# Optimization experiments

Measured on AMD Instinct MI355X. Metric: run time of the kernel, lower is better.

The kernel has to match this reference:

```python
import jax, jax.numpy as jnp
import numpy as np


def _chain_edges(n):
    # bidirectional chain edges + self loops (PyG GATConv add_self_loops=True default)
    src = np.concatenate([np.arange(n - 1), np.arange(1, n), np.arange(n)])
    dst = np.concatenate([np.arange(1, n), np.arange(n - 1), np.arange(n)])
    return jnp.asarray(src), jnp.asarray(dst)


def _gat(x, W, a_src, a_dst, bias, src, dst, n, heads, ch, concat):
    # x: [B, n, Fin]; PyG GATConv v1 math (lin has no bias, bias added post-agg)
    B = x.shape[0]
    xh = (x @ W).reshape(B, n, heads, ch)  # [B,n,h,c]
    es = jnp.einsum('bnhc,hc->bnh', xh, a_src)
    ed = jnp.einsum('bnhc,hc->bnh', xh, a_dst)
    e = jax.nn.leaky_relu(es[:, src] + ed[:, dst], 0.2)  # [B,E,h]
    e = jnp.moveaxis(e, 1, 0)                            # [E,B,h]
    m = jax.ops.segment_max(e, dst, num_segments=n)      # scatter-softmax over incoming edges
    w = jnp.exp(e - m[dst])
    denom = jax.ops.segment_sum(w, dst, num_segments=n)
    alpha = w / denom[dst]                               # [E,B,h]
    msgs = alpha[..., None] * jnp.moveaxis(xh[:, src], 1, 0)  # [E,B,h,c]
    out = jnp.moveaxis(jax.ops.segment_sum(msgs, dst, num_segments=n), 0, 1)  # [B,n,h,c]
    out = out.reshape(B, n, heads * ch) if concat else out.mean(axis=2)
    return out + bias


def _mlp(x, w1, b1, w2, b2, w3, b3):
    h = jax.nn.leaky_relu(x @ w1 + b1, 0.01)
    h = jax.nn.leaky_relu(h @ w2 + b2, 0.01)
    return h @ w3 + b3


def setup_inputs() -> dict:
    key = jax.random.key(0)
    ks = jax.random.split(key, 21)
    B, n, d_state, hid, da = 2048, 50, 64, 128, 4
    r = lambda k, shp, s: (jax.random.normal(k, shp, dtype=jnp.float32) * s)
    return {
        'state': r(ks[0], (B, n, d_state), 1.0),
        'W1': r(ks[1], (d_state, 2 * hid), 0.1), 'att_src1': r(ks[2], (2, hid), 0.1),
        'att_dst1': r(ks[3], (2, hid), 0.1), 'b1': r(ks[4], (2 * hid,), 0.02),
        'W2': r(ks[5], (2 * hid, hid), 0.1), 'att_src2': r(ks[6], (1, hid), 0.1),
        'att_dst2': r(ks[7], (1, hid), 0.1), 'b2': r(ks[8], (hid,), 0.02),
        'aw1': r(ks[9], (hid, 128), 0.1), 'ab1': r(ks[10], (128,), 0.02),
        'aw2': r(ks[11], (128, 128), 0.1), 'ab2': r(ks[12], (128,), 0.02),
        'aw3': r(ks[13], (128, da), 0.1), 'ab3': r(ks[14], (da,), 0.02),
        'vw1': r(ks[15], (hid, 128), 0.1), 'vb1': r(ks[16], (128,), 0.02),
        'vw2': r(ks[17], (128, 128), 0.1), 'vb2': r(ks[18], (128,), 0.02),
        'vw3': r(ks[19], (128, 1), 0.1), 'vb3': r(ks[20], (1,), 0.02),
    }


def reference(state, W1, att_src1, att_dst1, b1, W2, att_src2, att_dst2, b2,
              aw1, ab1, aw2, ab2, aw3, ab3, vw1, vb1, vw2, vb2, vw3, vb3):
    B, n, _ = state.shape
    src, dst = _chain_edges(n)
    x = jax.nn.gelu(_gat(state, W1, att_src1, att_dst1, b1, src, dst, n, 2, 128, True), approximate=False)
    x = jax.nn.gelu(_gat(x, W2, att_src2, att_dst2, b2, src, dst, n, 1, 128, False), approximate=False)
    graph_emb = x.mean(axis=1)                      # global_mean_pool over chain nodes
    value = _mlp(graph_emb, vw1, vb1, vw2, vb2, vw3, vb3)   # [B,1]
    mean = _mlp(x, aw1, ab1, aw2, ab2, aw3, ab3).reshape(B, -1)  # [B, n*d_action]
    return mean, value
```

## Files before the change

kernel.cpp:

```cpp
#include <hip/hip_runtime.h>

#define DI __device__ __forceinline__

typedef unsigned int uint32;
typedef unsigned short u16;
typedef __attribute__((ext_vector_type(8))) short s8v;
typedef __attribute__((ext_vector_type(4))) float f4v;

DI float lrelu(float x, float s){ return x > 0.f ? x : s*x; }
DI u16 f2bu(float f){ uint32 u = __float_as_uint(f); return (u16)((u + 0x7FFFu + ((u>>16)&1u)) >> 16); }
DI float fastrcp(float x){ float r; asm("v_rcp_f32 %0, %1" : "=v"(r) : "v"(x)); return r; }

DI float gelu_f(float x){
  const float z = fabsf(x) * 0.70710678118654752f;
  const float t = fastrcp(1.f + 0.3275911f*z);
  float p = 1.061405429f;
  p = p*t - 1.453152027f;
  p = p*t + 1.421413741f;
  p = p*t - 0.284496736f;
  p = p*t + 0.254829592f;
  p = p*t;
  const float e = __expf(-z*z);
  float er = 1.f - p*e;
  er = copysignf(er, x);
  return 0.5f*x*(1.f + er);
}

DI f4v mfma16(s8v a, s8v b, f4v c){
  return __builtin_amdgcn_mfma_f32_16x16x32_bf16(a, b, c, 0, 0, 0);
}

constexpr int NNODE = 50;
constexpr int NT = 512;
constexpr int SCS = 134;

constexpr int WS1  = 0;
constexpr int WS2  = 18432;
constexpr int WSA1 = 55296;
constexpr int WSA2 = 71680;
constexpr int WSTOT= 88064;

__global__ __launch_bounds__(256)
void ac_prep(const float* __restrict__ w1, const float* __restrict__ as1, const float* __restrict__ ad1,
             const float* __restrict__ w2, const float* __restrict__ as2, const float* __restrict__ ad2,
             const float* __restrict__ aw1, const float* __restrict__ aw2, u16* __restrict__ ws)
{
  const int T1 = 2*144*64, T2 = 144*256, T3 = 128*128;
  for (int t = blockIdx.x*blockDim.x + threadIdx.x; t < WSTOT; t += gridDim.x*blockDim.x){
    float v; int o;
    if (t < T1){
      int h = t / 9216, r = t - h*9216, n = r>>6, k = r&63;
      if (n < 128) v = w1[k*256 + h*128 + n];
      else if (n < 130){
        const float* av = ((n==129) ? ad1 : as1) + h*128;
        const float* wr = w1 + k*256 + h*128;
        float s = 0.f;
        for (int c=0;c<128;++c) s += wr[c]*av[c];
        v = s;
      } else v = 0.f;
      o = WS1 + h*9216 + n*64 + k;
    } else if (t < T1+T2){
      int j = t - T1, n = j>>8, k = j&255;
      if (n < 128) v = w2[k*128 + n];
      else if (n < 130){
        const float* av = (n==129) ? ad2 : as2;
        const float* wr = w2 + k*128;
        float s = 0.f;
        for (int c=0;c<128;++c) s += wr[c]*av[c];
        v = s;
      } else v = 0.f;
      o = WS2 + n*256 + k;
    } else if (t < T1+T2+T3){
      int j = t - T1 - T2, n = j>>7, k = j&127;
      v = aw1[k*128 + n];
      o = WSA1 + n*128 + k;
    } else {
      int j = t - T1 - T2 - T3, n = j>>7, k = j&127;
      v = aw2[k*128 + n];
      o = WSA2 + n*128 + k;
    }
    ws[o] = f2bu(v);
  }
}


__global__ __launch_bounds__(NT, 4)
void ac_main(const float* __restrict__ state,
             const float* __restrict__ b1, const float* __restrict__ b2,
             const float* __restrict__ ab1, const float* __restrict__ ab2,
             const float* __restrict__ aw3, const float* __restrict__ ab3,
             const float* __restrict__ vw1, const float* __restrict__ vb1,
             const float* __restrict__ vw2, const float* __restrict__ vb2,
             const float* __restrict__ vw3, const float* __restrict__ vb3,
             const u16* __restrict__ ws,
             float* __restrict__ out_mean, float* __restrict__ out_val)
{
  __shared__ __align__(16) float sm[18816];
  float* sc   = sm;
  u16*   pAb  = (u16*)(sm + 8576);
  u16*   pAb2 = pAb + 8192;
  u16*   pAs  = (u16*)(sm + 16768);
  float* geb4 = sm + 16768;
  float* geb  = sm + 17280;
  float* vh1  = sm + 17408;

  const int tid = threadIdx.x, b = blockIdx.x;
  const int wid = tid>>6, l15 = tid&15, g = (tid>>4)&3;

  {
    const float4* xb4 = (const float4*)(state + (size_t)b * (NNODE*64));
    for (int t = tid; t < 800; t += NT){
      float4 v = xb4[t];
      int i = t>>4, k0 = (t&15)*4;
      ushort4 u;
      u.x = f2bu(v.x); u.y = f2bu(v.y); u.z = f2bu(v.z); u.w = f2bu(v.w);
      *(ushort4*)(pAs + i*64 + (k0 ^ ((i&7)<<3))) = u;
    }
    for (int t = tid; t < 224; t += NT){
      int i = 50 + (t>>4), k0 = (t&15)*4;
      *(ushort4*)(pAs + i*64 + (k0 ^ ((i&7)<<3))) = (ushort4){0,0,0,0};
    }
  }
  __syncthreads();

  {
    s8v aS[4][2];
    #pragma unroll
    for (int mt=0;mt<4;++mt)
      #pragma unroll
      for (int ks=0;ks<2;++ks){
        int row = mt*16 + l15, c = ks*32 + g*8;
        aS[mt][ks] = *(const s8v*)(pAs + row*64 + (c ^ ((row&7)<<3)));
      }

    for (int h=0; h<2; ++h){
      for (int nt = wid; nt < 9; nt += 8){
        f4v acc[4];
        #pragma unroll
        for (int mt=0;mt<4;++mt) acc[mt] = (f4v){0.f,0.f,0.f,0.f};
        #pragma unroll
        for (int ks=0;ks<2;++ks){
          s8v bf = *(const s8v*)(ws + WS1 + h*9216 + (nt*16 + l15)*64 + ks*32 + g*8);
          #pragma unroll
          for (int mt=0;mt<4;++mt) acc[mt] = mfma16(aS[mt][ks], bf, acc[mt]);
        }
        const int col = nt*16 + l15;
        if (col < 130){
          #pragma unroll
          for (int mt=0;mt<4;++mt){
            const int r0 = mt*16 + g*4;
            #pragma unroll
            for (int r=0;r<4;++r) sc[(r0+r)*SCS + col] = acc[mt][r];
          }
        }
      }
      __syncthreads();

      {
        const int base_j = h*128;
        #pragma unroll 4
        for (int t=0; t<13; ++t){
          const int c = tid + t*NT;
          if (c < 6400){
            const int i = c >> 7, j = c & 127;
            const float edi = sc[i*SCS + 129];
            const float cur = sc[i*SCS + j];
            const float pv  = (i > 0)        ? sc[(i-1)*SCS + j] : 0.f;
            const float nx  = (i < NNODE-1)  ? sc[(i+1)*SCS + j] : 0.f;
            const float esf = lrelu(sc[i*SCS + 128] + edi, 0.2f);
            float m = esf, el = 0.f, er = 0.f;
            if (i > 0)       { el = lrelu(sc[(i-1)*SCS + 128] + edi, 0.2f); m = fmaxf(m, el); }
            if (i < NNODE-1) { er = lrelu(sc[(i+1)*SCS + 128] + edi, 0.2f); m = fmaxf(m, er); }
            const float wS = __expf(esf - m);
            const float wL = (i > 0)       ? __expf(el - m) : 0.f;
            const float wR = (i < NNODE-1) ? __expf(er - m) : 0.f;
            const float agg = (wL*pv + wS*cur + wR*nx) * fastrcp(wL+wS+wR);
            const float v = gelu_f(agg + b1[base_j + j]);
            const int jj = base_j + j;
            pAb[i*256 + (jj ^ ((i&7)<<3))] = f2bu(v);
          }
        }
      }
      __syncthreads();
    }
  }

  for (int nt = wid; nt < 9; nt += 8){
    f4v acc[4];
    #pragma unroll
    for (int mt=0;mt<4;++mt) acc[mt] = (f4v){0.f,0.f,0.f,0.f};
    #pragma unroll
    for (int ks=0;ks<8;++ks){
      s8v bf = *(const s8v*)(ws + WS2 + (nt*16 + l15)*256 + ks*32 + g*8);
      #pragma unroll
      for (int mt=0;mt<4;++mt){
        const int row = mt*16 + l15, c = ks*32 + g*8;
        s8v a = *(const s8v*)(pAb + row*256 + (c ^ ((row&7)<<3)));
        acc[mt] = mfma16(a, bf, acc[mt]);
      }
    }
    const int col = nt*16 + l15;
    if (col < 130){
      #pragma unroll
      for (int mt=0;mt<4;++mt){
        const int r0 = mt*16 + g*4;
        #pragma unroll
        for (int r=0;r<4;++r) sc[(r0+r)*SCS + col] = acc[mt][r];
      }
    }
  }
  __syncthreads();

  {
    const int q = tid>>7, j = tid&127;
    const int i0 = q*13, i1 = (i0+13 < NNODE) ? i0+13 : NNODE;
    const float bj = b2[j];
    float ps = 0.f;
    #pragma unroll 4
    for (int i = i0; i < i1; ++i){
      const float edi = sc[i*SCS + 129];
      const float cur = sc[i*SCS + j];
      const float pv  = (i > 0)       ? sc[(i-1)*SCS + j] : 0.f;
      const float nx  = (i < NNODE-1) ? sc[(i+1)*SCS + j] : 0.f;
      const float esf = lrelu(sc[i*SCS + 128] + edi, 0.2f);
      float m = esf, el = 0.f, er = 0.f;
      if (i > 0)       { el = lrelu(sc[(i-1)*SCS + 128] + edi, 0.2f); m = fmaxf(m, el); }
      if (i < NNODE-1) { er = lrelu(sc[(i+1)*SCS + 128] + edi, 0.2f); m = fmaxf(m, er); }
      const float wS = __expf(esf - m);
      const float wL = (i > 0)       ? __expf(el - m) : 0.f;
      const float wR = (i < NNODE-1) ? __expf(er - m) : 0.f;
      const float agg = (wL*pv + wS*cur + wR*nx) * fastrcp(wL+wS+wR);
      const float v = gelu_f(agg + bj);
      pAb[i*128 + (j ^ ((i&7)<<3))] = f2bu(v);
      ps += v;
    }
    geb4[q*128 + j] = ps;
  }
  __syncthreads();

  {
    const int nt = wid;
    f4v acc[4];
    #pragma unroll
    for (int mt=0;mt<4;++mt) acc[mt] = (f4v){0.f,0.f,0.f,0.f};
    #pragma unroll
    for (int ks=0;ks<4;++ks){
      s8v bf = *(const s8v*)(ws + WSA1 + (nt*16 + l15)*128 + ks*32 + g*8);
      #pragma unroll
      for (int mt=0;mt<4;++mt){
        const int row = mt*16 + l15, c = ks*32 + g*8;
        s8v a = *(const s8v*)(pAb + row*128 + (c ^ ((row&7)<<3)));
        acc[mt] = mfma16(a, bf, acc[mt]);
      }
    }
    const int col = nt*16 + l15;
    const float bj = ab1[col];
    #pragma unroll
    for (int mt=0;mt<4;++mt){
      #pragma unroll
      for (int r=0;r<4;++r){
        const int row = mt*16 + g*4 + r;
        const float v = lrelu(acc[mt][r] + bj, 0.01f);
        pAb2[row*128 + (col ^ ((row&7)<<3))] = f2bu(v);
      }
    }
    if (tid < 128)
      geb[tid] = (geb4[tid] + geb4[128+tid] + geb4[256+tid] + geb4[384+tid]) * 0.02f;
  }
  __syncthreads();

  {
    const int nt = wid;
    f4v acc[4];
    #pragma unroll
    for (int mt=0;mt<4;++mt) acc[mt] = (f4v){0.f,0.f,0.f,0.f};
    #pragma unroll
    for (int ks=0;ks<4;++ks){
      s8v bf = *(const s8v*)(ws + WSA2 + (nt*16 + l15)*128 + ks*32 + g*8);
      #pragma unroll
      for (int mt=0;mt<4;++mt){
        const int row = mt*16 + l15, c = ks*32 + g*8;
        s8v a = *(const s8v*)(pAb2 + row*128 + (c ^ ((row&7)<<3)));
        acc[mt] = mfma16(a, bf, acc[mt]);
      }
    }
    const int col = nt*16 + l15;
    #pragma unroll
    for (int mt=0;mt<4;++mt){
      const int r0 = mt*16 + g*4;
      #pragma unroll
      for (int r=0;r<4;++r) sc[(r0+r)*SCS + col] = acc[mt][r];
    }
  }
  __syncthreads();

  if (tid < 200){
    const int i = tid>>2, m = tid&3;
    const float* scr = sc + i*SCS;
    float s0=0.f,s1=0.f,s2=0.f,s3=0.f;
    #pragma unroll 4
    for (int k=0;k<128;k+=4){
      s0 += lrelu(scr[k  ]+ab2[k  ],0.01f)*aw3[(k  )*4+m];
      s1 += lrelu(scr[k+1]+ab2[k+1],0.01f)*aw3[(k+1)*4+m];
      s2 += lrelu(scr[k+2]+ab2[k+2],0.01f)*aw3[(k+2)*4+m];
      s3 += lrelu(scr[k+3]+ab2[k+3],0.01f)*aw3[(k+3)*4+m];
    }
    out_mean[(size_t)b*200 + i*4 + m] = (s0+s1)+(s2+s3) + ab3[m];
  } else if (tid >= 256 && tid < 384){
    const int j = tid - 256;
    float a0=0.f, a1=0.f;
    #pragma unroll 4
    for (int k=0;k<128;k+=2){
      a0 += geb[k  ]*vw1[(k  )*128 + j];
      a1 += geb[k+1]*vw1[(k+1)*128 + j];
    }
    vh1[j] = lrelu(a0+a1 + vb1[j], 0.01f);
  }
  __syncthreads();

  if (tid < 64){
    const int j = tid;
    float a0=0.f, c0=0.f;
    #pragma unroll 4
    for (int k=0;k<128;++k){
      const float gk = vh1[k];
      a0 += gk*vw2[k*128 + j];
      c0 += gk*vw2[k*128 + j + 64];
    }
    const float va = lrelu(a0 + vb2[j],    0.01f);
    const float vb = lrelu(c0 + vb2[j+64], 0.01f);
    float p = va*vw3[j] + vb*vw3[j+64];
    #pragma unroll
    for (int off=32; off>0; off>>=1) p += __shfl_down(p, off);
    if (j == 0) out_val[b] = p + vb3[0];
  }
}

extern "C" void kernel_launch(void* const* d_in, const int* in_sizes, int n_in,
                              void* d_out, int out_size, void* d_ws, size_t ws_size,
                              hipStream_t stream)
{
  const float* state = (const float*)d_in[0];
  const float* w1    = (const float*)d_in[1];
  const float* as1   = (const float*)d_in[2];
  const float* ad1   = (const float*)d_in[3];
  const float* b1_   = (const float*)d_in[4];
  const float* w2    = (const float*)d_in[5];
  const float* as2   = (const float*)d_in[6];
  const float* ad2   = (const float*)d_in[7];
  const float* b2_   = (const float*)d_in[8];
  const float* aw1   = (const float*)d_in[9];
  const float* ab1   = (const float*)d_in[10];
  const float* aw2   = (const float*)d_in[11];
  const float* ab2   = (const float*)d_in[12];
  const float* aw3   = (const float*)d_in[13];
  const float* ab3   = (const float*)d_in[14];
  const float* vw1   = (const float*)d_in[15];
  const float* vb1   = (const float*)d_in[16];
  const float* vw2   = (const float*)d_in[17];
  const float* vb2   = (const float*)d_in[18];
  const float* vw3   = (const float*)d_in[19];
  const float* vb3   = (const float*)d_in[20];

  const int B = in_sizes[0] / (NNODE * 64);
  float* out_mean = (float*)d_out;
  float* out_val  = out_mean + (size_t)B * 200;
  u16* ws = (u16*)d_ws;

  ac_prep<<<128, 256, 0, stream>>>(w1, as1, ad1, w2, as2, ad2, aw1, aw2, ws);
  ac_main<<<B, NT, 0, stream>>>(state, b1_, b2_, ab1, ab2, aw3, ab3,
                                vw1, vb1, vw2, vb2, vw3, vb3,
                                ws, out_mean, out_val);
}
```

Baseline: 153.3 us.

## Sliding-window GAT aggregation, MFMA final actor layer, merged value-head stages

Layer-1 GAT aggregation now gives each thread a contiguous range of nodes and slides a window over neighbour values, so each shared-memory value is loaded once instead of three times. The softmax max-subtraction is dropped in both layers. The last actor layer (128 to 4) is now a bf16 MFMA, with the bias and leaky-relu of the previous layer fused into its epilogue, replacing a scalar loop. The two value-MLP layers run in one wave without a block barrier between them, and the layer-1 A fragments are reloaded per head to reduce register pressure under waves_per_eu(4,4). Dropping the max-subtraction risks exp overflow on large logits, and the bf16 final layer adds rounding error.

Measured after the change: 157.3 us. 1.03x slower.

```diff
diff --git a/kernel.cpp b/kernel.cpp
--- a/kernel.cpp
+++ b/kernel.cpp
@@ -38,12 +38,14 @@
 constexpr int WS2  = 18432;
 constexpr int WSA1 = 55296;
 constexpr int WSA2 = 71680;
-constexpr int WSTOT= 88064;
+constexpr int WSA3 = 88064;
+constexpr int WSTOT= 90112;
 
 __global__ __launch_bounds__(256)
 void ac_prep(const float* __restrict__ w1, const float* __restrict__ as1, const float* __restrict__ ad1,
              const float* __restrict__ w2, const float* __restrict__ as2, const float* __restrict__ ad2,
-             const float* __restrict__ aw1, const float* __restrict__ aw2, u16* __restrict__ ws)
+             const float* __restrict__ aw1, const float* __restrict__ aw2, const float* __restrict__ aw3,
+             u16* __restrict__ ws)
 {
   const int T1 = 2*144*64, T2 = 144*256, T3 = 128*128;
   for (int t = blockIdx.x*blockDim.x + threadIdx.x; t < WSTOT; t += gridDim.x*blockDim.x){
@@ -74,21 +76,26 @@
       int j = t - T1 - T2, n = j>>7, k = j&127;
       v = aw1[k*128 + n];
       o = WSA1 + n*128 + k;
-    } else {
+    } else if (t < T1+T2+2*T3){
       int j = t - T1 - T2 - T3, n = j>>7, k = j&127;
       v = aw2[k*128 + n];
       o = WSA2 + n*128 + k;
+    } else {
+      int j = t - T1 - T2 - 2*T3, m = j>>7, k = j&127;
+      v = (m < 4) ? aw3[k*4 + m] : 0.f;
+      o = WSA3 + m*128 + k;
     }
     ws[o] = f2bu(v);
   }
 }
 
 
-__global__ __launch_bounds__(NT, 4)
+__global__ __launch_bounds__(NT)
+__attribute__((amdgpu_waves_per_eu(4, 4)))
 void ac_main(const float* __restrict__ state,
              const float* __restrict__ b1, const float* __restrict__ b2,
              const float* __restrict__ ab1, const float* __restrict__ ab2,
-             const float* __restrict__ aw3, const float* __restrict__ ab3,
+             const float* __restrict__ ab3,
              const float* __restrict__ vw1, const float* __restrict__ vb1,
              const float* __restrict__ vw2, const float* __restrict__ vb2,
              const float* __restrict__ vw3, const float* __restrict__ vb3,
@@ -123,17 +130,16 @@
   }
   __syncthreads();
 
-  {
-    s8v aS[4][2];
-    #pragma unroll
-    for (int mt=0;mt<4;++mt)
-      #pragma unroll
-      for (int ks=0;ks<2;++ks){
-        int row = mt*16 + l15, c = ks*32 + g*8;
-        aS[mt][ks] = *(const s8v*)(pAs + row*64 + (c ^ ((row&7)<<3)));
-      }
-
-    for (int h=0; h<2; ++h){
+  for (int h=0; h<2; ++h){
+    {
+      s8v aS[4][2];
+      #pragma unroll
+      for (int mt=0;mt<4;++mt)
+        #pragma unroll
+        for (int ks=0;ks<2;++ks){
+          int row = mt*16 + l15, c = ks*32 + g*8;
+          aS[mt][ks] = *(const s8v*)(pAs + row*64 + (c ^ ((row&7)<<3)));
+        }
       for (int nt = wid; nt < 9; nt += 8){
         f4v acc[4];
         #pragma unroll
@@ -154,35 +160,33 @@
           }
         }
       }
-      __syncthreads();
-
-      {
-        const int base_j = h*128;
-        #pragma unroll 4
-        for (int t=0; t<13; ++t){
-          const int c = tid + t*NT;
-          if (c < 6400){
-            const int i = c >> 7, j = c & 127;
-            const float edi = sc[i*SCS + 129];
-            const float cur = sc[i*SCS + j];
-            const float pv  = (i > 0)        ? sc[(i-1)*SCS + j] : 0.f;
-            const float nx  = (i < NNODE-1)  ? sc[(i+1)*SCS + j] : 0.f;
-            const float esf = lrelu(sc[i*SCS + 128] + edi, 0.2f);
-            float m = esf, el = 0.f, er = 0.f;
-            if (i > 0)       { el = lrelu(sc[(i-1)*SCS + 128] + edi, 0.2f); m = fmaxf(m, el); }
-            if (i < NNODE-1) { er = lrelu(sc[(i+1)*SCS + 128] + edi, 0.2f); m = fmaxf(m, er); }
-            const float wS = __expf(esf - m);
-            const float wL = (i > 0)       ? __expf(el - m) : 0.f;
-            const float wR = (i < NNODE-1) ? __expf(er - m) : 0.f;
-            const float agg = (wL*pv + wS*cur + wR*nx) * fastrcp(wL+wS+wR);
-            const float v = gelu_f(agg + b1[base_j + j]);
-            const int jj = base_j + j;
-            pAb[i*256 + (jj ^ ((i&7)<<3))] = f2bu(v);
-          }
-        }
-      }
-      __syncthreads();
-    }
+    }
+    __syncthreads();
+
+    {
+      const int q = tid>>7, j = tid&127, jj = h*128 + j;
+      const int i0 = q*13, i1 = (i0+13 < NNODE) ? i0+13 : NNODE;
+      const float bj = b1[jj];
+      float pv  = (i0 > 0) ? sc[(i0-1)*SCS + j]   : 0.f;
+      float cur = sc[i0*SCS + j];
+      float esm = (i0 > 0) ? sc[(i0-1)*SCS + 128] : 0.f;
+      float es0 = sc[i0*SCS + 128];
+      #pragma unroll 4
+      for (int i = i0; i < i1; ++i){
+        const float nx  = (i < NNODE-1) ? sc[(i+1)*SCS + j]   : 0.f;
+        const float esp = (i < NNODE-1) ? sc[(i+1)*SCS + 128] : 0.f;
+        const float edi = sc[i*SCS + 129];
+        const float wS = __expf(lrelu(es0 + edi, 0.2f));
+        const float wL = (i > 0)       ? __expf(lrelu(esm + edi, 0.2f)) : 0.f;
+        const float wR = (i < NNODE-1) ? __expf(lrelu(esp + edi, 0.2f)) : 0.f;
+        const float rs = fastrcp(wL + wS + wR);
+        const float agg = (wL*pv + wS*cur + wR*nx) * rs;
+        const float v = gelu_f(agg + bj);
+        pAb[i*256 + (jj ^ ((i&7)<<3))] = f2bu(v);
+        pv = cur; cur = nx; esm = es0; es0 = esp;
+      }
+    }
+    __syncthreads();
   }
 
   for (int nt = wid; nt < 9; nt += 8){
@@ -216,23 +220,24 @@
     const int i0 = q*13, i1 = (i0+13 < NNODE) ? i0+13 : NNODE;
     const float bj = b2[j];
     float ps = 0.f;
+    float pv  = (i0 > 0) ? sc[(i0-1)*SCS + j]   : 0.f;
+    float cur = sc[i0*SCS + j];
+    float esm = (i0 > 0) ? sc[(i0-1)*SCS + 128] : 0.f;
+    float es0 = sc[i0*SCS + 128];
     #pragma unroll 4
     for (int i = i0; i < i1; ++i){
+      const float nx  = (i < NNODE-1) ? sc[(i+1)*SCS + j]   : 0.f;
+      const float esp = (i < NNODE-1) ? sc[(i+1)*SCS + 128] : 0.f;
       const float edi = sc[i*SCS + 129];
-      const float cur = sc[i*SCS + j];
-      const float pv  = (i > 0)       ? sc[(i-1)*SCS + j] : 0.f;
-      const float nx  = (i < NNODE-1) ? sc[(i+1)*SCS + j] : 0.f;
-      const float esf = lrelu(sc[i*SCS + 128] + edi, 0.2f);
-      float m = esf, el = 0.f, er = 0.f;
-      if (i > 0)       { el = lrelu(sc[(i-1)*SCS + 128] + edi, 0.2f); m = fmaxf(m, el); }
-      if (i < NNODE-1) { er = lrelu(sc[(i+1)*SCS + 128] + edi, 0.2f); m = fmaxf(m, er); }
-      const float wS = __expf(esf - m);
-      const float wL = (i > 0)       ? __expf(el - m) : 0.f;
-      const float wR = (i < NNODE-1) ? __expf(er - m) : 0.f;
-      const float agg = (wL*pv + wS*cur + wR*nx) * fastrcp(wL+wS+wR);
+      const float wS = __expf(lrelu(es0 + edi, 0.2f));
+      const float wL = (i > 0)       ? __expf(lrelu(esm + edi, 0.2f)) : 0.f;
+      const float wR = (i < NNODE-1) ? __expf(lrelu(esp + edi, 0.2f)) : 0.f;
+      const float rs = fastrcp(wL + wS + wR);
+      const float agg = (wL*pv + wS*cur + wR*nx) * rs;
       const float v = gelu_f(agg + bj);
       pAb[i*128 + (j ^ ((i&7)<<3))] = f2bu(v);
       ps += v;
+      pv = cur; cur = nx; esm = es0; es0 = esp;
     }
     geb4[q*128 + j] = ps;
   }
@@ -285,50 +290,59 @@
       }
     }
     const int col = nt*16 + l15;
+    const float bj = ab2[col];
     #pragma unroll
     for (int mt=0;mt<4;++mt){
-      const int r0 = mt*16 + g*4;
-      #pragma unroll
-      for (int r=0;r<4;++r) sc[(r0+r)*SCS + col] = acc[mt][r];
-    }
-  }
-  __syncthreads();
-
-  if (tid < 200){
-    const int i = tid>>2, m = tid&3;
-    const float* scr = sc + i*SCS;
-    float s0=0.f,s1=0.f,s2=0.f,s3=0.f;
-    #pragma unroll 4
-    for (int k=0;k<128;k+=4){
-      s0 += lrelu(scr[k  ]+ab2[k  ],0.01f)*aw3[(k  )*4+m];
-      s1 += lrelu(scr[k+1]+ab2[k+1],0.01f)*aw3[(k+1)*4+m];
-      s2 += lrelu(scr[k+2]+ab2[k+2],0.01f)*aw3[(k+2)*4+m];
-      s3 += lrelu(scr[k+3]+ab2[k+3],0.01f)*aw3[(k+3)*4+m];
-    }
-    out_mean[(size_t)b*200 + i*4 + m] = (s0+s1)+(s2+s3) + ab3[m];
-  } else if (tid >= 256 && tid < 384){
-    const int j = tid - 256;
+      #pragma unroll
+      for (int r=0;r<4;++r){
+        const int row = mt*16 + g*4 + r;
+        const float v = lrelu(acc[mt][r] + bj, 0.01f);
+        pAb[row*128 + (col ^ ((row&7)<<3))] = f2bu(v);
+      }
+    }
+  }
+  __syncthreads();
+
+  if (wid < 4){
+    const int mt = wid;
+    f4v acc = (f4v){0.f,0.f,0.f,0.f};
+    #pragma unroll
+    for (int ks=0;ks<4;++ks){
+      s8v bf = *(const s8v*)(ws + WSA3 + l15*128 + ks*32 + g*8);
+      const int row = mt*16 + l15, c = ks*32 + g*8;
+      s8v a = *(const s8v*)(pAb + row*128 + (c ^ ((row&7)<<3)));
+      acc = mfma16(a, bf, acc);
+    }
+    if (l15 < 4){
+      const float bj = ab3[l15];
+      #pragma unroll
+      for (int r=0;r<4;++r){
+        const int row = mt*16 + g*4 + r;
+        if (row < NNODE) out_mean[(size_t)b*200 + row*4 + l15] = acc[r] + bj;
+      }
+    }
+  } else if (wid == 4){
+    const int j = tid & 63;
     float a0=0.f, a1=0.f;
     #pragma unroll 4
-    for (int k=0;k<128;k+=2){
-      a0 += geb[k  ]*vw1[(k  )*128 + j];
-      a1 += geb[k+1]*vw1[(k+1)*128 + j];
-    }
-    vh1[j] = lrelu(a0+a1 + vb1[j], 0.01f);
-  }
-  __syncthreads();
-
-  if (tid < 64){
-    const int j = tid;
-    float a0=0.f, c0=0.f;
+    for (int k=0;k<128;++k){
+      const float gk = geb[k];
+      a0 += gk*vw1[k*128 + j];
+      a1 += gk*vw1[k*128 + j + 64];
+    }
+    vh1[j]      = lrelu(a0 + vb1[j],    0.01f);
+    vh1[j + 64] = lrelu(a1 + vb1[j+64], 0.01f);
+    asm volatile("s_waitcnt lgkmcnt(0)" ::: "memory");
+    __builtin_amdgcn_sched_barrier(0);
+    float c0=0.f, c1=0.f;
     #pragma unroll 4
     for (int k=0;k<128;++k){
-      const float gk = vh1[k];
-      a0 += gk*vw2[k*128 + j];
-      c0 += gk*vw2[k*128 + j + 64];
-    }
-    const float va = lrelu(a0 + vb2[j],    0.01f);
-    const float vb = lrelu(c0 + vb2[j+64], 0.01f);
+      const float hk = vh1[k];
+      c0 += hk*vw2[k*128 + j];
+      c1 += hk*vw2[k*128 + j + 64];
+    }
+    const float va = lrelu(c0 + vb2[j],    0.01f);
+    const float vb = lrelu(c1 + vb2[j+64], 0.01f);
     float p = va*vw3[j] + vb*vw3[j+64];
     #pragma unroll
     for (int off=32; off>0; off>>=1) p += __shfl_down(p, off);
@@ -367,8 +381,8 @@
   float* out_val  = out_mean + (size_t)B * 200;
   u16* ws = (u16*)d_ws;
 
-  ac_prep<<<128, 256, 0, stream>>>(w1, as1, ad1, w2, as2, ad2, aw1, aw2, ws);
-  ac_main<<<B, NT, 0, stream>>>(state, b1_, b2_, ab1, ab2, aw3, ab3,
+  ac_prep<<<128, 256, 0, stream>>>(w1, as1, ad1, w2, as2, ad2, aw1, aw2, aw3, ws);
+  ac_main<<<B, NT, 0, stream>>>(state, b1_, b2_, ab1, ab2, ab3,
                                 vw1, vb1, vw2, vb2, vw3, vb3,
                                 ws, out_mean, out_val);
 }
```
